# Kernel tuning notes

Hardware: AMD Instinct MI355X
Metric: run time of the kernel (lower is better)

## Reference

```python
import jax, jax.numpy as jnp
import numpy as np

N_HEAD = 16

def setup_inputs() -> dict:
    key = jax.random.key(0)
    ks = jax.random.split(key, 5)
    B, S, D = 2, 2048, 1024
    x = jax.random.normal(ks[0], (B, S, D), dtype=jnp.float32)
    w_attn = jax.random.normal(ks[1], (3 * D, D), dtype=jnp.float32) * 0.02
    b_attn = jax.random.normal(ks[2], (3 * D,), dtype=jnp.float32) * 0.02
    w_proj = jax.random.normal(ks[3], (D, D), dtype=jnp.float32) * 0.02
    b_proj = jax.random.normal(ks[4], (D,), dtype=jnp.float32) * 0.02
    return {"x": x, "w_attn": w_attn, "b_attn": b_attn, "w_proj": w_proj, "b_proj": b_proj}

def reference(x, w_attn, b_attn, w_proj, b_proj):
    B, S, D = x.shape
    H = N_HEAD
    hd = D // H
    # QKV projection (nn.Linear: x @ W^T + b)
    qkv = x @ w_attn.T + b_attn  # [B, S, 3D]
    q, k, v = jnp.split(qkv, 3, axis=2)
    q = q.reshape(B, S, H, hd).transpose(0, 2, 1, 3)  # [B, H, S, hd]
    k = k.reshape(B, S, H, hd).transpose(0, 2, 1, 3)
    v = v.reshape(B, S, H, hd).transpose(0, 2, 1, 3)
    scale = 1.0 / jnp.sqrt(jnp.asarray(hd, dtype=x.dtype))
    attn = jnp.einsum("bhqd,bhkd->bhqk", q, k) * scale  # [B, H, S, S]
    causal = jnp.tril(jnp.ones((S, S), dtype=bool))
    attn = jnp.where(causal[None, None], attn, -jnp.inf)
    attn = jax.nn.softmax(attn, axis=-1)
    y = jnp.einsum("bhqk,bhkd->bhqd", attn, v)  # [B, H, S, hd]
    y = y.transpose(0, 2, 1, 3).reshape(B, S, D)
    return y @ w_proj.T + b_proj
```

## Files before the change

### kernel.cpp

```cpp
#include <hip/hip_runtime.h>
#include <hip/hip_bf16.h>

#define S_LEN 2048
#define DMODEL 1024
#define NHEAD 16
#define HD 64

typedef short short8 __attribute__((ext_vector_type(8)));
typedef short short4_t __attribute__((ext_vector_type(4)));
typedef float f32x4 __attribute__((ext_vector_type(4)));

#define GLOAD_LDS16(gp, lp)                                        \
    __builtin_amdgcn_global_load_lds(                              \
        (__attribute__((address_space(1))) void*)(gp),             \
        (__attribute__((address_space(3))) void*)(lp), 16, 0, 0)

__device__ inline unsigned short f2bf(float f) {
    union { float f; unsigned int u; } c;
    c.f = f;
    unsigned int r = c.u + 0x7fffu + ((c.u >> 16) & 1u);
    return (unsigned short)(r >> 16);
}

__global__ __launch_bounds__(256) void cast3_f32_bf16(
    const float* __restrict__ x, const float* __restrict__ wa,
    const float* __restrict__ wp,
    short* __restrict__ xb, short* __restrict__ wab, short* __restrict__ wpb)
{
    const int i = blockIdx.x * 256 + threadIdx.x;
    const float* src;
    short* dst;
    if (i < 524288)      { src = x  + (size_t)i * 8;            dst = xb  + (size_t)i * 8; }
    else if (i < 917504) { src = wa + (size_t)(i - 524288) * 8; dst = wab + (size_t)(i - 524288) * 8; }
    else                 { src = wp + (size_t)(i - 917504) * 8; dst = wpb + (size_t)(i - 917504) * 8; }
    float4 a = ((const float4*)src)[0];
    float4 b = ((const float4*)src)[1];
    short8 o;
    o[0] = (short)f2bf(a.x); o[1] = (short)f2bf(a.y);
    o[2] = (short)f2bf(a.z); o[3] = (short)f2bf(a.w);
    o[4] = (short)f2bf(b.x); o[5] = (short)f2bf(b.y);
    o[6] = (short)f2bf(b.z); o[7] = (short)f2bf(b.w);
    *(short8*)dst = o;
}

template<bool QKV>
__global__ __launch_bounds__(256) void gemm_mfma(
    const short* __restrict__ A, const short* __restrict__ W,
    const float* __restrict__ bias, float* __restrict__ C,
    int N, int K,
    short* __restrict__ qo, short* __restrict__ ko, short* __restrict__ vo)
{
    __shared__ __align__(16) short Ash[2][128 * 64];
    __shared__ __align__(16) short Bsh[2][128 * 64];

    const int tid = threadIdx.x;
    const int l = tid & 63;
    const int wid = tid >> 6;
    const int wr = wid >> 1, wc = wid & 1;
    const int n0 = blockIdx.x << 7, m0 = blockIdx.y << 7;

    const short* Abase = A + (size_t)m0 * K;
    const short* Wbase = W + (size_t)n0 * K;

    f32x4 acc[4][4];
    #pragma unroll
    for (int i = 0; i < 4; ++i)
        #pragma unroll
        for (int j = 0; j < 4; ++j)
            acc[i][j] = (f32x4)0.0f;

    int rrow[4], scol[4];
    #pragma unroll
    for (int i = 0; i < 4; ++i) {
        int chunk = i * 256 + tid;
        rrow[i] = chunk >> 3;
        scol[i] = ((chunk & 7) ^ (rrow[i] & 7)) << 3;
    }

    auto stage = [&](int buf, int k0) {
        #pragma unroll
        for (int i = 0; i < 4; ++i) {
            GLOAD_LDS16(Abase + (size_t)rrow[i] * K + k0 + scol[i],
                        &Ash[buf][(i * 256 + wid * 64) * 8]);
            GLOAD_LDS16(Wbase + (size_t)rrow[i] * K + k0 + scol[i],
                        &Bsh[buf][(i * 256 + wid * 64) * 8]);
        }
    };

    auto compute = [&](int buf) {
        #pragma unroll
        for (int kk = 0; kk < 2; ++kk) {
            short8 af[4], bf[4];
            const int slotg = (kk << 2) + (l >> 4);
            #pragma unroll
            for (int mi = 0; mi < 4; ++mi) {
                const int row = wr * 64 + mi * 16 + (l & 15);
                af[mi] = *(const short8*)&Ash[buf][row * 64 + ((slotg ^ (row & 7)) << 3)];
            }
            #pragma unroll
            for (int ni = 0; ni < 4; ++ni) {
                const int row = wc * 64 + ni * 16 + (l & 15);
                bf[ni] = *(const short8*)&Bsh[buf][row * 64 + ((slotg ^ (row & 7)) << 3)];
            }
            #pragma unroll
            for (int mi = 0; mi < 4; ++mi)
                #pragma unroll
                for (int ni = 0; ni < 4; ++ni)
                    acc[mi][ni] = __builtin_amdgcn_mfma_f32_16x16x32_bf16(
                        af[mi], bf[ni], acc[mi][ni], 0, 0, 0);
        }
    };

    const int NT = K >> 6;
    stage(0, 0);
    __syncthreads();
    int cur = 0;
    for (int kt = 0; kt < NT; ++kt) {
        if (kt + 1 < NT) stage(cur ^ 1, (kt + 1) << 6);
        compute(cur);
        __syncthreads();
        cur ^= 1;
    }

    #pragma unroll
    for (int ni = 0; ni < 4; ++ni) {
        const int col = n0 + wc * 64 + ni * 16 + (l & 15);
        const float bv = bias[col];
        if (QKV) {
            const int part = col >> 10;
            const int h = (col >> 6) & 15;
            const int e = col & 63;
            short* __restrict__ dst = part == 0 ? qo : (part == 1 ? ko : vo);
            #pragma unroll
            for (int mi = 0; mi < 4; ++mi) {
                #pragma unroll
                for (int r = 0; r < 4; ++r) {
                    int row = m0 + wr * 64 + mi * 16 + ((l >> 4) << 2) + r;
                    int b = row >> 11, s = row & (S_LEN - 1);
                    dst[((size_t)(b * NHEAD + h) * S_LEN + s) * HD + e] =
                        (short)f2bf(acc[mi][ni][r] + bv);
                }
            }
        } else {
            #pragma unroll
            for (int mi = 0; mi < 4; ++mi) {
                #pragma unroll
                for (int r = 0; r < 4; ++r) {
                    int row = m0 + wr * 64 + mi * 16 + ((l >> 4) << 2) + r;
                    C[(size_t)row * N + col] = acc[mi][ni][r] + bv;
                }
            }
        }
    }
}

__global__ __launch_bounds__(256) void transpose_v(
    const short* __restrict__ vin, short* __restrict__ vout)
{
    __shared__ short t[64][72];
    const int tid = threadIdx.x;
    const int bh = blockIdx.x >> 5;
    const int s0 = (blockIdx.x & 31) << 6;
    const size_t ibase = (size_t)bh * S_LEN * HD;
    const size_t obase = (size_t)bh * HD * S_LEN;
    const int r = tid >> 3, c8 = (tid & 7) << 3;

    #pragma unroll
    for (int p = 0; p < 2; ++p) {
        short8 v = *(const short8*)&vin[ibase + (size_t)(s0 + r + p * 32) * HD + c8];
        *(short8*)&t[r + p * 32][c8] = v;
    }
    __syncthreads();
    #pragma unroll
    for (int p = 0; p < 2; ++p) {
        const int e = r + p * 32;
        short8 o;
        #pragma unroll
        for (int i = 0; i < 8; ++i) o[i] = t[c8 + i][e];
        *(short8*)&vout[obase + (size_t)e * S_LEN + s0 + c8] = o;
    }
}

__global__ __launch_bounds__(256) void flash_attn_mfma(
    const short* __restrict__ q, const short* __restrict__ k,
    const short* __restrict__ vt, short* __restrict__ yb)
{
    __shared__ __align__(16) short Ks[2][64 * 64];
    __shared__ __align__(16) short Vs[2][64 * 64];

    const int tid = threadIdx.x;
    const int l = tid & 63;
    const int w = tid >> 6;
    const int h4 = l >> 4;
    const int c15 = l & 15;
    const int bid = blockIdx.x;
    const int qt = 31 - (bid >> 5);
    const int bh = bid & 31;
    const int q0 = qt << 6;
    const int myq = q0 + (w << 4) + c15;

    const size_t kbase = (size_t)bh * S_LEN * HD;
    const size_t vbase = (size_t)bh * HD * S_LEN;

    short8 qf[2];
    {
        const short* qrow = q + kbase + (size_t)myq * HD;
        qf[0] = *(const short8*)(qrow + (h4 << 3));
        qf[1] = *(const short8*)(qrow + 32 + (h4 << 3));
    }

    f32x4 accO[4];
    #pragma unroll
    for (int i = 0; i < 4; ++i) accO[i] = (f32x4)0.0f;
    float mr = -1e30f, lr = 0.0f;

    const int sr = tid >> 3, slotL = tid & 7;

    auto stageKV = [&](int buf, int kn) {
        #pragma unroll
        for (int p = 0; p < 2; ++p) {
            const int row = sr + p * 32;
            const int ss = (slotL ^ (row & 7)) << 3;
            GLOAD_LDS16(k + kbase + (size_t)(kn + row) * HD + ss,
                        &Ks[buf][(p * 256 + w * 64) * 8]);
            GLOAD_LDS16(vt + vbase + (size_t)row * S_LEN + kn + ss,
                        &Vs[buf][(p * 256 + w * 64) * 8]);
        }
    };

    const int ntiles = qt + 1;
    stageKV(0, 0);
    __syncthreads();
    int cur = 0;

    for (int t = 0; t < ntiles; ++t) {
        if (t + 1 < ntiles) stageKV(cur ^ 1, (t + 1) << 6);

        f32x4 sacc[4];
        #pragma unroll
        for (int nt = 0; nt < 4; ++nt) sacc[nt] = (f32x4)0.0f;
        #pragma unroll
        for (int c = 0; c < 2; ++c) {
            const int kof = (c << 5) + (h4 << 3);
            #pragma unroll
            for (int nt = 0; nt < 4; ++nt) {
                const int keyrow = nt * 16 + c15;
                const short8 kf = *(const short8*)&Ks[cur][keyrow * 64 + (kof ^ ((keyrow & 7) << 3))];
                sacc[nt] = __builtin_amdgcn_mfma_f32_16x16x32_bf16(kf, qf[c], sacc[nt], 0, 0, 0);
            }
        }

        float p16[16];
        const bool diag = (t == qt);
        #pragma unroll
        for (int nt = 0; nt < 4; ++nt)
            #pragma unroll
            for (int r = 0; r < 4; ++r) {
                float v = sacc[nt][r] * 0.125f;
                if (diag && (nt * 16 + (h4 << 2) + r > (w << 4) + c15))
                    v = -1e30f;
                p16[nt * 4 + r] = v;
            }

        float mx = p16[0];
        #pragma unroll
        for (int i = 1; i < 16; ++i) mx = fmaxf(mx, p16[i]);
        mx = fmaxf(mx, __shfl_xor(mx, 16, 64));
        mx = fmaxf(mx, __shfl_xor(mx, 32, 64));
        if (!__all(mx <= mr)) {
            const float mnew = fmaxf(mr, mx);
            const float alpha = __expf(mr - mnew);
            mr = mnew;
            lr *= alpha;
            #pragma unroll
            for (int et = 0; et < 4; ++et) accO[et] *= alpha;
        }
        float rs = 0.0f;
        #pragma unroll
        for (int i = 0; i < 16; ++i) {
            p16[i] = __expf(p16[i] - mr);
            rs += p16[i];
        }
        rs += __shfl_xor(rs, 16, 64);
        rs += __shfl_xor(rs, 32, 64);
        lr += rs;

        short8 pb[2];
        #pragma unroll
        for (int c = 0; c < 2; ++c)
            #pragma unroll
            for (int i = 0; i < 8; ++i)
                pb[c][i] = (short)f2bf(p16[8 * c + i]);

        #pragma unroll
        for (int c = 0; c < 2; ++c) {
            const int ch = (c << 2) + (h4 >> 1);
            const int halfo = (h4 & 1) << 2;
            #pragma unroll
            for (int et = 0; et < 4; ++et) {
                const int e = (et << 4) + c15;
                const int rb = e << 6;
                const int sw = e & 7;
                const short4_t va = *(const short4_t*)&Vs[cur][rb + ((ch ^ sw) << 3) + halfo];
                const short4_t vb = *(const short4_t*)&Vs[cur][rb + (((ch + 2) ^ sw) << 3) + halfo];
                const short8 vf = {va[0], va[1], va[2], va[3], vb[0], vb[1], vb[2], vb[3]};
                accO[et] = __builtin_amdgcn_mfma_f32_16x16x32_bf16(vf, pb[c], accO[et], 0, 0, 0);
            }
        }

        __syncthreads();
        cur ^= 1;
    }

    const int bq = bh >> 4, hh = bh & 15;
    const float inv = 1.0f / lr;
    short* orow = yb + ((size_t)bq * S_LEN + myq) * DMODEL + hh * HD;
    #pragma unroll
    for (int et = 0; et < 4; ++et) {
        short4_t o;
        #pragma unroll
        for (int r = 0; r < 4; ++r) o[r] = (short)f2bf(accO[et][r] * inv);
        *(short4_t*)&orow[(et << 4) + (h4 << 2)] = o;
    }
}

extern "C" void kernel_launch(void* const* d_in, const int* in_sizes, int n_in,
                              void* d_out, int out_size, void* d_ws, size_t ws_size,
                              hipStream_t stream) {
    const float* x      = (const float*)d_in[0];
    const float* w_attn = (const float*)d_in[1];
    const float* b_attn = (const float*)d_in[2];
    const float* w_proj = (const float*)d_in[3];
    const float* b_proj = (const float*)d_in[4];
    float* out = (float*)d_out;

    const int B = 2;
    const int M = B * S_LEN;

    char* wsb = (char*)d_ws;
    short* qw  = (short*)(wsb);
    short* kw  = (short*)(wsb + (8u << 20));
    short* vw  = (short*)(wsb + (16u << 20));
    short* vtw = (short*)(wsb + (24u << 20));
    short* xb  = (short*)(wsb + (32u << 20));
    short* yb  = (short*)(wsb + (32u << 20));
    short* wab = (short*)(wsb + (40u << 20));
    short* wpb = (short*)(wsb + (46u << 20));

    cast3_f32_bf16<<<dim3(4096), 256, 0, stream>>>(x, w_attn, w_proj, xb, wab, wpb);

    dim3 g1(3 * DMODEL / 128, M / 128);
    gemm_mfma<true><<<g1, 256, 0, stream>>>(xb, wab, b_attn, nullptr,
                                            3 * DMODEL, DMODEL, qw, kw, vw);

    transpose_v<<<dim3(2 * NHEAD * (S_LEN / 64)), 256, 0, stream>>>(vw, vtw);

    flash_attn_mfma<<<dim3(2 * NHEAD * (S_LEN / 64)), 256, 0, stream>>>(qw, kw, vtw, yb);

    dim3 g3(DMODEL / 128, M / 128);
    gemm_mfma<false><<<g3, 256, 0, stream>>>(yb, wpb, b_proj, out,
                                             DMODEL, DMODEL,
                                             nullptr, nullptr, nullptr);
}
```

Before: 196.5 us.

## Vectorize GEMM epilogue stores and permute V-transpose layout for single LDS reads

The GEMM swaps MFMA operand order so each lane holds four consecutive columns, which lets the bias be read as a float4 and the outputs be written as packed 4-wide stores instead of scalar ones. The V transpose writes a permuted key order so flash attention can fetch each V fragment with one 16-byte LDS read instead of two 8-byte reads. Flash attention also drops the double-buffered global-to-LDS async copy in favour of register prefetch with single LDS buffers. That halves LDS use, which may allow more blocks per CU, but adds a second barrier per tile and staging through registers.

```diff
diff --git a/kernel.cpp b/kernel.cpp
--- a/kernel.cpp
+++ b/kernel.cpp
@@ -57,6 +57,7 @@
     const int l = tid & 63;
     const int wid = tid >> 6;
     const int wr = wid >> 1, wc = wid & 1;
+    const int c15 = l & 15, h4 = l >> 4;
     const int n0 = blockIdx.x << 7, m0 = blockIdx.y << 7;
 
     const short* Abase = A + (size_t)m0 * K;
@@ -91,15 +92,15 @@
         #pragma unroll
         for (int kk = 0; kk < 2; ++kk) {
             short8 af[4], bf[4];
-            const int slotg = (kk << 2) + (l >> 4);
+            const int slotg = (kk << 2) + h4;
             #pragma unroll
             for (int mi = 0; mi < 4; ++mi) {
-                const int row = wr * 64 + mi * 16 + (l & 15);
+                const int row = wr * 64 + mi * 16 + c15;
                 af[mi] = *(const short8*)&Ash[buf][row * 64 + ((slotg ^ (row & 7)) << 3)];
             }
             #pragma unroll
             for (int ni = 0; ni < 4; ++ni) {
-                const int row = wc * 64 + ni * 16 + (l & 15);
+                const int row = wc * 64 + ni * 16 + c15;
                 bf[ni] = *(const short8*)&Bsh[buf][row * 64 + ((slotg ^ (row & 7)) << 3)];
             }
             #pragma unroll
@@ -107,7 +108,7 @@
                 #pragma unroll
                 for (int ni = 0; ni < 4; ++ni)
                     acc[mi][ni] = __builtin_amdgcn_mfma_f32_16x16x32_bf16(
-                        af[mi], bf[ni], acc[mi][ni], 0, 0, 0);
+                        bf[ni], af[mi], acc[mi][ni], 0, 0, 0);
         }
     };
 
@@ -124,31 +125,34 @@
 
     #pragma unroll
     for (int ni = 0; ni < 4; ++ni) {
-        const int col = n0 + wc * 64 + ni * 16 + (l & 15);
-        const float bv = bias[col];
+        const int colb = n0 + wc * 64 + ni * 16 + (h4 << 2);
+        const float4 b4 = *(const float4*)&bias[colb];
         if (QKV) {
-            const int part = col >> 10;
-            const int h = (col >> 6) & 15;
-            const int e = col & 63;
+            const int part = colb >> 10;
+            const int h = (colb >> 6) & 15;
+            const int e = colb & 63;
             short* __restrict__ dst = part == 0 ? qo : (part == 1 ? ko : vo);
             #pragma unroll
             for (int mi = 0; mi < 4; ++mi) {
-                #pragma unroll
-                for (int r = 0; r < 4; ++r) {
-                    int row = m0 + wr * 64 + mi * 16 + ((l >> 4) << 2) + r;
-                    int b = row >> 11, s = row & (S_LEN - 1);
-                    dst[((size_t)(b * NHEAD + h) * S_LEN + s) * HD + e] =
-                        (short)f2bf(acc[mi][ni][r] + bv);
-                }
+                const int row = m0 + wr * 64 + mi * 16 + c15;
+                const int b = row >> 11, s = row & (S_LEN - 1);
+                short4_t o;
+                o[0] = (short)f2bf(acc[mi][ni][0] + b4.x);
+                o[1] = (short)f2bf(acc[mi][ni][1] + b4.y);
+                o[2] = (short)f2bf(acc[mi][ni][2] + b4.z);
+                o[3] = (short)f2bf(acc[mi][ni][3] + b4.w);
+                *(short4_t*)&dst[((size_t)(b * NHEAD + h) * S_LEN + s) * HD + e] = o;
             }
         } else {
             #pragma unroll
             for (int mi = 0; mi < 4; ++mi) {
-                #pragma unroll
-                for (int r = 0; r < 4; ++r) {
-                    int row = m0 + wr * 64 + mi * 16 + ((l >> 4) << 2) + r;
-                    C[(size_t)row * N + col] = acc[mi][ni][r] + bv;
-                }
+                const int row = m0 + wr * 64 + mi * 16 + c15;
+                float4 o;
+                o.x = acc[mi][ni][0] + b4.x;
+                o.y = acc[mi][ni][1] + b4.y;
+                o.z = acc[mi][ni][2] + b4.z;
+                o.w = acc[mi][ni][3] + b4.w;
+                *(float4*)&C[(size_t)row * N + colb] = o;
             }
         }
     }
@@ -171,13 +175,15 @@
         *(short8*)&t[r + p * 32][c8] = v;
     }
     __syncthreads();
+    const int P0 = (c8 & 32) | ((c8 & 8) << 1) | ((c8 & 16) >> 2);
     #pragma unroll
     for (int p = 0; p < 2; ++p) {
         const int e = r + p * 32;
-        short8 o;
-        #pragma unroll
-        for (int i = 0; i < 8; ++i) o[i] = t[c8 + i][e];
-        *(short8*)&vout[obase + (size_t)e * S_LEN + s0 + c8] = o;
+        short4_t lo, hi;
+        #pragma unroll
+        for (int i = 0; i < 4; ++i) { lo[i] = t[c8 + i][e]; hi[i] = t[c8 + 4 + i][e]; }
+        *(short4_t*)&vout[obase + (size_t)e * S_LEN + s0 + P0] = lo;
+        *(short4_t*)&vout[obase + (size_t)e * S_LEN + s0 + P0 + 8] = hi;
     }
 }
 
@@ -185,8 +191,8 @@
     const short* __restrict__ q, const short* __restrict__ k,
     const short* __restrict__ vt, short* __restrict__ yb)
 {
-    __shared__ __align__(16) short Ks[2][64 * 64];
-    __shared__ __align__(16) short Vs[2][64 * 64];
+    __shared__ __align__(16) short Ks[64 * 64];
+    __shared__ __align__(16) short Vs[64 * 64];
 
     const int tid = threadIdx.x;
     const int l = tid & 63;
@@ -214,27 +220,33 @@
     for (int i = 0; i < 4; ++i) accO[i] = (f32x4)0.0f;
     float mr = -1e30f, lr = 0.0f;
 
-    const int sr = tid >> 3, slotL = tid & 7;
-
-    auto stageKV = [&](int buf, int kn) {
+    const int srow0 = tid >> 3, scol = tid & 7;
+    short8 kreg[2], vreg[2];
+    #pragma unroll
+    for (int p = 0; p < 2; ++p) {
+        kreg[p] = *(const short8*)(k + kbase + (size_t)(srow0 + p * 32) * HD + scol * 8);
+        vreg[p] = *(const short8*)(vt + vbase + (size_t)(srow0 + p * 32) * S_LEN + scol * 8);
+    }
+
+    const int ntiles = qt + 1;
+    for (int t = 0; t < ntiles; ++t) {
+        __syncthreads();
         #pragma unroll
         for (int p = 0; p < 2; ++p) {
-            const int row = sr + p * 32;
-            const int ss = (slotL ^ (row & 7)) << 3;
-            GLOAD_LDS16(k + kbase + (size_t)(kn + row) * HD + ss,
-                        &Ks[buf][(p * 256 + w * 64) * 8]);
-            GLOAD_LDS16(vt + vbase + (size_t)row * S_LEN + kn + ss,
-                        &Vs[buf][(p * 256 + w * 64) * 8]);
-        }
-    };
-
-    const int ntiles = qt + 1;
-    stageKV(0, 0);
-    __syncthreads();
-    int cur = 0;
-
-    for (int t = 0; t < ntiles; ++t) {
-        if (t + 1 < ntiles) stageKV(cur ^ 1, (t + 1) << 6);
+            const int row = srow0 + p * 32;
+            const int sc = (scol ^ (row & 7)) << 3;
+            *(short8*)&Ks[row * 64 + sc] = kreg[p];
+            *(short8*)&Vs[row * 64 + sc] = vreg[p];
+        }
+        __syncthreads();
+        if (t + 1 < ntiles) {
+            const int kn = (t + 1) << 6;
+            #pragma unroll
+            for (int p = 0; p < 2; ++p) {
+                kreg[p] = *(const short8*)(k + kbase + (size_t)(kn + srow0 + p * 32) * HD + scol * 8);
+                vreg[p] = *(const short8*)(vt + vbase + (size_t)(srow0 + p * 32) * S_LEN + kn + scol * 8);
+            }
+        }
 
         f32x4 sacc[4];
         #pragma unroll
@@ -245,7 +257,7 @@
             #pragma unroll
             for (int nt = 0; nt < 4; ++nt) {
                 const int keyrow = nt * 16 + c15;
-                const short8 kf = *(const short8*)&Ks[cur][keyrow * 64 + (kof ^ ((keyrow & 7) << 3))];
+                const short8 kf = *(const short8*)&Ks[keyrow * 64 + (kof ^ ((keyrow & 7) << 3))];
                 sacc[nt] = __builtin_amdgcn_mfma_f32_16x16x32_bf16(kf, qf[c], sacc[nt], 0, 0, 0);
             }
         }
@@ -294,22 +306,14 @@
 
         #pragma unroll
         for (int c = 0; c < 2; ++c) {
-            const int ch = (c << 2) + (h4 >> 1);
-            const int halfo = (h4 & 1) << 2;
+            const int fs = (c << 2) + h4;
             #pragma unroll
             for (int et = 0; et < 4; ++et) {
                 const int e = (et << 4) + c15;
-                const int rb = e << 6;
-                const int sw = e & 7;
-                const short4_t va = *(const short4_t*)&Vs[cur][rb + ((ch ^ sw) << 3) + halfo];
-                const short4_t vb = *(const short4_t*)&Vs[cur][rb + (((ch + 2) ^ sw) << 3) + halfo];
-                const short8 vf = {va[0], va[1], va[2], va[3], vb[0], vb[1], vb[2], vb[3]};
+                const short8 vf = *(const short8*)&Vs[(e << 6) + ((fs ^ (e & 7)) << 3)];
                 accO[et] = __builtin_amdgcn_mfma_f32_16x16x32_bf16(vf, pb[c], accO[et], 0, 0, 0);
             }
         }
-
-        __syncthreads();
-        cur ^= 1;
     }
 
     const int bq = bh >> 4, hh = bh & 15;
```

Result: faster. 191.1 us (-2.8%).
